# Optimization experiments

Measured on AMD Instinct MI355X. Metric: run time of the kernel, lower is better.

Reference implementation:

```python
import jax, jax.numpy as jnp
import numpy as np

N = 50000      # nodes
F = 128        # in_features
OUT = 128      # out_features
E = 600000     # edges per adjacency (avg degree 12)
J = 2
BN_EPS = 1e-5


def setup_inputs() -> dict:
    key = jax.random.key(0)
    ks = jax.random.split(key, 10)
    x = jax.random.normal(ks[0], (N, F), dtype=jnp.float32)
    rows0 = jax.random.randint(ks[1], (E,), 0, N, dtype=jnp.int32)
    cols0 = jax.random.randint(ks[2], (E,), 0, N, dtype=jnp.int32)
    vals0 = jax.random.uniform(ks[3], (E,), dtype=jnp.float32)
    rows1 = jax.random.randint(ks[4], (E,), 0, N, dtype=jnp.int32)
    cols1 = jax.random.randint(ks[5], (E,), 0, N, dtype=jnp.int32)
    vals1 = jax.random.uniform(ks[6], (E,), dtype=jnp.float32)
    # Linear(J*F, OUT) params, torch default init U(-1/sqrt(fan_in), 1/sqrt(fan_in))
    lim = 1.0 / np.sqrt(J * F)
    W_fc = jax.random.uniform(ks[7], (OUT, J * F), dtype=jnp.float32, minval=-lim, maxval=lim)
    b_fc = jax.random.uniform(ks[8], (OUT,), dtype=jnp.float32, minval=-lim, maxval=lim)
    gamma = jnp.ones((OUT,), dtype=jnp.float32)
    beta = jnp.zeros((OUT,), dtype=jnp.float32)
    return {"x": x, "rows0": rows0, "cols0": cols0, "vals0": vals0,
            "rows1": rows1, "cols1": cols1, "vals1": vals1,
            "W_fc": W_fc, "b_fc": b_fc, "gamma": gamma, "beta": beta}


def _spmm(rows, cols, vals, x):
    # sparse [N,N] @ dense [N,F]: gather source features, weight, scatter-add to rows
    msgs = vals[:, None] * x[cols]                      # [E, F]
    return jax.ops.segment_sum(msgs, rows, num_segments=x.shape[0])  # [N, F]


def reference(x, rows0, cols0, vals0, rows1, cols1, vals1, W_fc, b_fc, gamma, beta):
    h = jnp.concatenate([_spmm(rows0, cols0, vals0, x),
                         _spmm(rows1, cols1, vals1, x)], axis=1)  # [N, J*F]
    y = h @ W_fc.T + b_fc                                         # [N, OUT]
    # BatchNorm1d (training mode: batch stats, biased variance)
    mean = jnp.mean(y, axis=0)
    var = jnp.mean((y - mean) ** 2, axis=0)
    return (y - mean) * jax.lax.rsqrt(var + BN_EPS) * gamma + beta
```

## Files before the change

### kernel.cpp

```cpp
#include <hip/hip_runtime.h>

#define N_NODES 50000
#define F_IN 128
#define OUT_F 128
#define JF 256
#define EDGES 600000
#define BN_EPS 1e-5f
#define MAXDEG 48
#define NPART 8
#define PART_ROWS 6250
#define CHUNK_E 2048
#define NCHUNK 586

#define SCAT_B (NPART * NCHUNK)
#define CONVX_B 6250
#define CONVW_B 32
#define BUILD_B (SCAT_B + CONVX_B + CONVW_B)
#define ROWS_PB 32
#define GATH_B 1563
#define GEMM_ROWS 32
#define GEMM_B 1563
#define HPAD 50048
#define NCOPY 16

typedef __attribute__((ext_vector_type(8))) short short8;
typedef __attribute__((ext_vector_type(4))) float floatx4;
typedef __attribute__((ext_vector_type(4))) unsigned short ushortx4;

static __device__ __forceinline__ unsigned short f2bf(float f) {
    unsigned int x = __float_as_uint(f);
    unsigned int r = (x + 0x7fffu + ((x >> 16) & 1u)) >> 16;
    return (unsigned short)r;
}
static __device__ __forceinline__ float bflo(unsigned int p) { return __uint_as_float(p << 16); }
static __device__ __forceinline__ float bfhi(unsigned int p) { return __uint_as_float(p & 0xffff0000u); }

__global__ __launch_bounds__(256) void build_kernel(
    const int* __restrict__ rows0, const int* __restrict__ cols0, const float* __restrict__ vals0,
    const int* __restrict__ rows1, const int* __restrict__ cols1, const float* __restrict__ vals1,
    int* __restrict__ cnt0, int* __restrict__ cnt1,
    unsigned int* __restrict__ pe0, unsigned int* __restrict__ pe1,
    const floatx4* __restrict__ x4, ushortx4* __restrict__ xb4,
    const float* __restrict__ W, uint2* __restrict__ Wb2)
{
    int bid = blockIdx.x;
    int tid = threadIdx.x;
    if (bid < SCAT_B) {
        unsigned part = (unsigned)(bid & (NPART - 1));
        int c0 = (bid >> 3) * CHUNK_E;

        bool pure0 = (c0 + CHUNK_E <= EDGES);
        bool pure1 = (c0 >= EDGES) && (c0 + CHUNK_E <= 2 * EDGES);
        if (pure0 || pure1) {
            const int*   rows = pure1 ? rows1 : rows0;
            const int*   cols = pure1 ? cols1 : cols0;
            const float* vals = pure1 ? vals1 : vals0;
            int*          cnt = pure1 ? cnt1 : cnt0;
            unsigned int*  pe = pure1 ? pe1 : pe0;
            int eb = pure1 ? c0 - EDGES : c0;
            #pragma unroll
            for (int g = 0; g < 2; ++g) {
                int e = eb + g * 1024 + tid * 4;
                int4 rv = *(const int4*)(rows + e);
                int rr[4] = {rv.x, rv.y, rv.z, rv.w};
                #pragma unroll
                for (int j = 0; j < 4; ++j) {
                    int r = rr[j];
                    if ((unsigned)r / (unsigned)PART_ROWS == part) {
                        int ee = e + j;
                        int c = cols[ee];
                        float v = vals[ee];
                        int p = atomicAdd(&cnt[r], 1);
                        if (p < MAXDEG)
                            pe[(size_t)r * MAXDEG + p] = ((unsigned int)c << 16) | f2bf(v);
                    }
                }
            }
        } else {
            for (int i = 0; i < CHUNK_E / 256; ++i) {
                int e = c0 + i * 256 + tid;
                if (e < 2 * EDGES) {
                    bool s1 = e >= EDGES;
                    int ee = s1 ? e - EDGES : e;
                    int r = s1 ? rows1[ee] : rows0[ee];
                    if ((unsigned)r / (unsigned)PART_ROWS == part) {
                        int c = s1 ? cols1[ee] : cols0[ee];
                        float v = s1 ? vals1[ee] : vals0[ee];
                        int* cnt = s1 ? cnt1 : cnt0;
                        unsigned int* pe = s1 ? pe1 : pe0;
                        int p = atomicAdd(&cnt[r], 1);
                        if (p < MAXDEG)
                            pe[(size_t)r * MAXDEG + p] = ((unsigned int)c << 16) | f2bf(v);
                    }
                }
            }
        }
    } else if (bid < SCAT_B + CONVX_B) {
        int i = (bid - SCAT_B) * 256 + tid;
        floatx4 v = __builtin_nontemporal_load(&x4[i]);
        ushortx4 o;
        o.x = f2bf(v.x); o.y = f2bf(v.y); o.z = f2bf(v.z); o.w = f2bf(v.w);
        __builtin_nontemporal_store(o, &xb4[i]);
    } else {
        int i = (bid - SCAT_B - CONVX_B) * 256 + tid;
        int col = i >> 6, l = i & 63;
        const float* wr = W + (size_t)col * JF;
        float a0 = wr[2 * l], a1 = wr[2 * l + 1];
        float b0 = wr[128 + 2 * l], b1 = wr[128 + 2 * l + 1];
        uint2 o;
        o.x = (unsigned int)f2bf(a0) | ((unsigned int)f2bf(a1) << 16);
        o.y = (unsigned int)f2bf(b0) | ((unsigned int)f2bf(b1) << 16);
        Wb2[col * 64 + l] = o;
    }
}

static __device__ __forceinline__ void rec_u(
    unsigned int q, int lane,
    const unsigned int* __restrict__ xb32, float& A0, float& A1)
{
    unsigned int xv = xb32[(q >> 16) * 64 + lane];
    float vv = __uint_as_float(q << 16);
    A0 += vv * bflo(xv);
    A1 += vv * bfhi(xv);
}
static __device__ __forceinline__ void rec_m(
    unsigned int q, bool on, int lane,
    const unsigned int* __restrict__ xb32, float& A0, float& A1)
{
    unsigned int idx = on ? (q >> 16) : 0u;
    float vv = on ? __uint_as_float(q << 16) : 0.0f;
    unsigned int xv = xb32[idx * 64 + lane];
    A0 += vv * bflo(xv);
    A1 += vv * bfhi(xv);
}

__global__ __launch_bounds__(256, 8) void gather_kernel(
    const unsigned int* __restrict__ xb32,
    const int* __restrict__ cnt0, const unsigned int* __restrict__ pe0,
    const int* __restrict__ cnt1, const unsigned int* __restrict__ pe1,
    uint2* __restrict__ hb)
{
    __shared__ uint4 recs[2][ROWS_PB][6];
    __shared__ int   lcnt[2][ROWS_PB];

    int tid = threadIdx.x;
    int lane = tid & 63;
    int w = tid >> 6;
    int wu = __builtin_amdgcn_readfirstlane(w);
    int row0 = blockIdx.x * ROWS_PB;

    {
        int idx = tid;
        #pragma unroll
        for (int pass = 0; pass < 2; ++pass) {
            if (idx < 384) {
                int lr = idx / 12;
                int rem = idx - lr * 12;
                int side = rem >= 6;
                int g = rem - side * 6;
                int r = row0 + lr; if (r >= N_NODES) r = N_NODES - 1;
                const unsigned int* pe = side ? pe1 : pe0;
                recs[side][lr][g] = *(const uint4*)(pe + (size_t)r * MAXDEG + g * 4);
            }
            idx += 256;
        }
        if (tid < 64) {
            int side = tid >= ROWS_PB;
            int lr = tid & (ROWS_PB - 1);
            int r = row0 + lr;
            int d = 0;
            if (r < N_NODES) d = (side ? cnt1 : cnt0)[r];
            if (d > MAXDEG) d = MAXDEG;
            lcnt[side][lr] = d;
        }
    }
    __syncthreads();

    for (int rr = 0; rr < 8; ++rr) {
        int lr = wu * 8 + rr;
        int r = row0 + lr;
        int d0 = __builtin_amdgcn_readfirstlane(lcnt[0][lr]);
        int d1 = __builtin_amdgcn_readfirstlane(lcnt[1][lr]);

        float aL0 = 0.f, aL1 = 0.f, aR0 = 0.f, aR1 = 0.f;

        #pragma unroll
        for (int g = 0; g < 6; ++g) {
            if (g * 4 < d0) {
                uint4 q = recs[0][lr][g];
                rec_u(q.x, lane, xb32, aL0, aL1);
                rec_m(q.y, g * 4 + 1 < d0, lane, xb32, aL0, aL1);
                rec_m(q.z, g * 4 + 2 < d0, lane, xb32, aL0, aL1);
                rec_m(q.w, g * 4 + 3 < d0, lane, xb32, aL0, aL1);
            }
        }
        #pragma unroll
        for (int g = 0; g < 6; ++g) {
            if (g * 4 < d1) {
                uint4 q = recs[1][lr][g];
                rec_u(q.x, lane, xb32, aR0, aR1);
                rec_m(q.y, g * 4 + 1 < d1, lane, xb32, aR0, aR1);
                rec_m(q.z, g * 4 + 2 < d1, lane, xb32, aR0, aR1);
                rec_m(q.w, g * 4 + 3 < d1, lane, xb32, aR0, aR1);
            }
        }
        if (d0 > 24 && r < N_NODES)
            for (int p = 24; p < d0; ++p)
                rec_u(pe0[(size_t)r * MAXDEG + p], lane, xb32, aL0, aL1);
        if (d1 > 24 && r < N_NODES)
            for (int p = 24; p < d1; ++p)
                rec_u(pe1[(size_t)r * MAXDEG + p], lane, xb32, aR0, aR1);

        uint2 o;
        o.x = (unsigned int)f2bf(aL0) | ((unsigned int)f2bf(aL1) << 16);
        o.y = (unsigned int)f2bf(aR0) | ((unsigned int)f2bf(aR1) << 16);
        hb[(size_t)(row0 + lr) * 64 + lane] = o;
    }
}

__global__ __launch_bounds__(256, 6) void gemm_kernel(
    const char* __restrict__ hb,
    const ushort* __restrict__ Wb,
    const float* __restrict__ bias,
    float* __restrict__ y, float* __restrict__ stats)
{
    __shared__ float lstat[256];

    int tid = threadIdx.x;
    int lane = tid & 63;
    int w = tid >> 6;
    int row0 = blockIdx.x * GEMM_ROWS + (w & 1) * 16;
    int cbase = (w >> 1) * 64;

    lstat[tid] = 0.f;
    __syncthreads();

    int colb = lane & 15;
    int kg = lane >> 4;
    const char* abase = hb + (size_t)(row0 + colb) * 512 + kg * 16;

    floatx4 acc[4];
    #pragma unroll
    for (int c = 0; c < 4; ++c) acc[c] = (floatx4){0.f, 0.f, 0.f, 0.f};

    #pragma unroll
    for (int k0 = 0; k0 < 8; ++k0) {
        short8 a = *(const short8*)(abase + k0 * 64);
        #pragma unroll
        for (int c = 0; c < 4; ++c) {
            short8 b = *(const short8*)(Wb + (size_t)(cbase + c * 16 + colb) * 256 + k0 * 32 + kg * 8);
            acc[c] = __builtin_amdgcn_mfma_f32_16x16x32_bf16(a, b, acc[c], 0, 0, 0);
        }
    }

    #pragma unroll
    for (int c = 0; c < 4; ++c) {
        int col = cbase + c * 16 + colb;
        float bv = bias[col];
        float s = 0.f, s2 = 0.f;
        #pragma unroll
        for (int q = 0; q < 4; ++q) {
            int row = row0 + kg * 4 + q;
            if (row < N_NODES) {
                float val = acc[c][q] + bv;
                y[(size_t)row * OUT_F + col] = val;
                s += val; s2 += val * val;
            }
        }
        atomicAdd(&lstat[col], s);
        atomicAdd(&lstat[128 + col], s2);
    }
    __syncthreads();
    float* sdst = stats + (size_t)(blockIdx.x & (NCOPY - 1)) * 256;
    atomicAdd(&sdst[tid], lstat[tid]);
}

__global__ void bn_prep(const float* __restrict__ stats,
                        const float* __restrict__ gamma,
                        const float* __restrict__ beta,
                        float* __restrict__ ss)
{
    int o = threadIdx.x;
    if (o >= OUT_F) return;
    float s = 0.f, s2 = 0.f;
    #pragma unroll
    for (int c = 0; c < NCOPY; ++c) {
        s  += stats[c * 256 + o];
        s2 += stats[c * 256 + 128 + o];
    }
    float inv_n = 1.0f / (float)N_NODES;
    float mean = s * inv_n;
    float var  = s2 * inv_n - mean * mean;
    float sc = rsqrtf(var + BN_EPS) * gamma[o];
    ss[o] = sc;
    ss[OUT_F + o] = beta[o] - mean * sc;
}

__global__ __launch_bounds__(256) void bn_apply(
    float* __restrict__ y, const float* __restrict__ ss)
{
    size_t i = (size_t)blockIdx.x * blockDim.x + threadIdx.x;
    size_t total = (size_t)N_NODES * OUT_F / 4;
    if (i >= total) return;

    int c4 = (int)(i & (OUT_F / 4 - 1));
    float4 v  = ((const float4*)y)[i];
    float4 sc = ((const float4*)ss)[c4];
    float4 sh = ((const float4*)(ss + OUT_F))[c4];
    v.x = v.x * sc.x + sh.x;
    v.y = v.y * sc.y + sh.y;
    v.z = v.z * sc.z + sh.z;
    v.w = v.w * sc.w + sh.w;
    ((float4*)y)[i] = v;
}

extern "C" void kernel_launch(void* const* d_in, const int* in_sizes, int n_in,
                              void* d_out, int out_size, void* d_ws, size_t ws_size,
                              hipStream_t stream)
{
    const float* x     = (const float*)d_in[0];
    const int*   rows0 = (const int*)  d_in[1];
    const int*   cols0 = (const int*)  d_in[2];
    const float* vals0 = (const float*)d_in[3];
    const int*   rows1 = (const int*)  d_in[4];
    const int*   cols1 = (const int*)  d_in[5];
    const float* vals1 = (const float*)d_in[6];
    const float* W     = (const float*)d_in[7];
    const float* b     = (const float*)d_in[8];
    const float* gamma = (const float*)d_in[9];
    const float* beta  = (const float*)d_in[10];

    float* y = (float*)d_out;

    ushort* xb = (ushort*)d_ws;
    ushort* Wb = xb + (size_t)N_NODES * F_IN;
    unsigned int* pe0 = (unsigned int*)(Wb + OUT_F * JF);
    unsigned int* pe1 = pe0 + (size_t)N_NODES * MAXDEG;
    uint2* hb = (uint2*)(pe1 + (size_t)N_NODES * MAXDEG);
    int* cnt0 = (int*)(hb + (size_t)HPAD * 64);
    int* cnt1 = cnt0 + N_NODES;
    float* stats = (float*)(cnt1 + N_NODES);
    float* ss    = stats + NCOPY * 256;

    hipMemsetAsync(cnt0, 0,
                   (2 * (size_t)N_NODES + NCOPY * 256) * sizeof(int),
                   stream);

    build_kernel<<<BUILD_B, 256, 0, stream>>>(
        rows0, cols0, vals0, rows1, cols1, vals1,
        cnt0, cnt1, pe0, pe1,
        (const floatx4*)x, (ushortx4*)xb, W, (uint2*)Wb);

    gather_kernel<<<GATH_B, 256, 0, stream>>>(
        (const unsigned int*)xb, cnt0, pe0, cnt1, pe1, hb);

    gemm_kernel<<<GEMM_B, 256, 0, stream>>>(
        (const char*)hb, Wb, b, y, stats);

    bn_prep<<<1, 128, 0, stream>>>(stats, gamma, beta, ss);
    bn_apply<<<CONVX_B, 256, 0, stream>>>(y, ss);
}
```

Baseline: 170.2 us.

## Pre-pack edges into compact arrays before partitioned scatter; fuse BN prep into apply

Adds a prep pass that packs row indices into 16-bit values and packs col/val pairs into one 32-bit word per edge. A separate scatter kernel then has each of the 8 partition blocks read the compact row array, so the repeated row scans across partitions read half the bytes and the col/val loads become a single word. The one-block bn_prep launch is merged into bn_apply: every block recomputes the scale and shift in shared memory. This costs an extra kernel launch and an extra pass writing and reading the packed arrays, and each bn block redoes the small stats reduction.

```diff
diff --git a/kernel.cpp b/kernel.cpp
--- a/kernel.cpp
+++ b/kernel.cpp
@@ -12,10 +12,12 @@
 #define CHUNK_E 2048
 #define NCHUNK 586
 
-#define SCAT_B (NPART * NCHUNK)
+#define RPACK_B 586
+#define EV_B 1172
 #define CONVX_B 6250
 #define CONVW_B 32
-#define BUILD_B (SCAT_B + CONVX_B + CONVW_B)
+#define PREP_B (RPACK_B + EV_B + CONVX_B + CONVW_B)
+#define SCAT_B (NPART * NCHUNK)
 #define ROWS_PB 32
 #define GATH_B 1563
 #define GEMM_ROWS 32
@@ -24,6 +26,7 @@
 #define NCOPY 16
 
 typedef __attribute__((ext_vector_type(8))) short short8;
+typedef __attribute__((ext_vector_type(8))) unsigned short ushortx8;
 typedef __attribute__((ext_vector_type(4))) float floatx4;
 typedef __attribute__((ext_vector_type(4))) unsigned short ushortx4;
 
@@ -35,74 +38,52 @@
 static __device__ __forceinline__ float bflo(unsigned int p) { return __uint_as_float(p << 16); }
 static __device__ __forceinline__ float bfhi(unsigned int p) { return __uint_as_float(p & 0xffff0000u); }
 
-__global__ __launch_bounds__(256) void build_kernel(
+__global__ __launch_bounds__(256) void prep_kernel(
     const int* __restrict__ rows0, const int* __restrict__ cols0, const float* __restrict__ vals0,
     const int* __restrict__ rows1, const int* __restrict__ cols1, const float* __restrict__ vals1,
-    int* __restrict__ cnt0, int* __restrict__ cnt1,
-    unsigned int* __restrict__ pe0, unsigned int* __restrict__ pe1,
+    unsigned short* __restrict__ rpack, unsigned int* __restrict__ ev,
     const floatx4* __restrict__ x4, ushortx4* __restrict__ xb4,
     const float* __restrict__ W, uint2* __restrict__ Wb2)
 {
     int bid = blockIdx.x;
     int tid = threadIdx.x;
-    if (bid < SCAT_B) {
-        unsigned part = (unsigned)(bid & (NPART - 1));
-        int c0 = (bid >> 3) * CHUNK_E;
-
-        bool pure0 = (c0 + CHUNK_E <= EDGES);
-        bool pure1 = (c0 >= EDGES) && (c0 + CHUNK_E <= 2 * EDGES);
-        if (pure0 || pure1) {
-            const int*   rows = pure1 ? rows1 : rows0;
-            const int*   cols = pure1 ? cols1 : cols0;
-            const float* vals = pure1 ? vals1 : vals0;
-            int*          cnt = pure1 ? cnt1 : cnt0;
-            unsigned int*  pe = pure1 ? pe1 : pe0;
-            int eb = pure1 ? c0 - EDGES : c0;
-            #pragma unroll
-            for (int g = 0; g < 2; ++g) {
-                int e = eb + g * 1024 + tid * 4;
-                int4 rv = *(const int4*)(rows + e);
-                int rr[4] = {rv.x, rv.y, rv.z, rv.w};
-                #pragma unroll
-                for (int j = 0; j < 4; ++j) {
-                    int r = rr[j];
-                    if ((unsigned)r / (unsigned)PART_ROWS == part) {
-                        int ee = e + j;
-                        int c = cols[ee];
-                        float v = vals[ee];
-                        int p = atomicAdd(&cnt[r], 1);
-                        if (p < MAXDEG)
-                            pe[(size_t)r * MAXDEG + p] = ((unsigned int)c << 16) | f2bf(v);
-                    }
-                }
-            }
-        } else {
-            for (int i = 0; i < CHUNK_E / 256; ++i) {
-                int e = c0 + i * 256 + tid;
-                if (e < 2 * EDGES) {
-                    bool s1 = e >= EDGES;
-                    int ee = s1 ? e - EDGES : e;
-                    int r = s1 ? rows1[ee] : rows0[ee];
-                    if ((unsigned)r / (unsigned)PART_ROWS == part) {
-                        int c = s1 ? cols1[ee] : cols0[ee];
-                        float v = s1 ? vals1[ee] : vals0[ee];
-                        int* cnt = s1 ? cnt1 : cnt0;
-                        unsigned int* pe = s1 ? pe1 : pe0;
-                        int p = atomicAdd(&cnt[r], 1);
-                        if (p < MAXDEG)
-                            pe[(size_t)r * MAXDEG + p] = ((unsigned int)c << 16) | f2bf(v);
-                    }
-                }
-            }
-        }
-    } else if (bid < SCAT_B + CONVX_B) {
-        int i = (bid - SCAT_B) * 256 + tid;
+    if (bid < RPACK_B) {
+        int e0 = bid * 2048 + tid * 8;
+        if (e0 < 2 * EDGES) {
+            bool s1 = e0 >= EDGES;
+            const int* rows = s1 ? rows1 : rows0;
+            int eb = s1 ? e0 - EDGES : e0;
+            int4 a = *(const int4*)(rows + eb);
+            int4 b = *(const int4*)(rows + eb + 4);
+            ushortx8 o;
+            o.s0 = (unsigned short)a.x; o.s1 = (unsigned short)a.y;
+            o.s2 = (unsigned short)a.z; o.s3 = (unsigned short)a.w;
+            o.s4 = (unsigned short)b.x; o.s5 = (unsigned short)b.y;
+            o.s6 = (unsigned short)b.z; o.s7 = (unsigned short)b.w;
+            *(ushortx8*)(rpack + e0) = o;
+        }
+    } else if (bid < RPACK_B + EV_B) {
+        int e0 = (bid - RPACK_B) * 1024 + tid * 4;
+        if (e0 < 2 * EDGES) {
+            bool s1 = e0 >= EDGES;
+            int eb = s1 ? e0 - EDGES : e0;
+            int4 c = *(const int4*)((s1 ? cols1 : cols0) + eb);
+            float4 v = *(const float4*)((s1 ? vals1 : vals0) + eb);
+            uint4 o;
+            o.x = ((unsigned)c.x << 16) | f2bf(v.x);
+            o.y = ((unsigned)c.y << 16) | f2bf(v.y);
+            o.z = ((unsigned)c.z << 16) | f2bf(v.z);
+            o.w = ((unsigned)c.w << 16) | f2bf(v.w);
+            *(uint4*)(ev + e0) = o;
+        }
+    } else if (bid < RPACK_B + EV_B + CONVX_B) {
+        int i = (bid - RPACK_B - EV_B) * 256 + tid;
         floatx4 v = __builtin_nontemporal_load(&x4[i]);
         ushortx4 o;
         o.x = f2bf(v.x); o.y = f2bf(v.y); o.z = f2bf(v.z); o.w = f2bf(v.w);
         __builtin_nontemporal_store(o, &xb4[i]);
     } else {
-        int i = (bid - SCAT_B - CONVX_B) * 256 + tid;
+        int i = (bid - RPACK_B - EV_B - CONVX_B) * 256 + tid;
         int col = i >> 6, l = i & 63;
         const float* wr = W + (size_t)col * JF;
         float a0 = wr[2 * l], a1 = wr[2 * l + 1];
@@ -111,6 +92,33 @@
         o.x = (unsigned int)f2bf(a0) | ((unsigned int)f2bf(a1) << 16);
         o.y = (unsigned int)f2bf(b0) | ((unsigned int)f2bf(b1) << 16);
         Wb2[col * 64 + l] = o;
+    }
+}
+
+__global__ __launch_bounds__(256) void scat_kernel(
+    const unsigned short* __restrict__ rpack, const unsigned int* __restrict__ ev,
+    int* __restrict__ cnt0, int* __restrict__ cnt1,
+    unsigned int* __restrict__ pe0, unsigned int* __restrict__ pe1)
+{
+    unsigned part = (unsigned)(blockIdx.x & (NPART - 1));
+    int e0 = (blockIdx.x >> 3) * CHUNK_E + threadIdx.x * 8;
+    if (e0 >= 2 * EDGES) return;
+
+    bool s1 = e0 >= EDGES;
+    int* __restrict__ cnt = s1 ? cnt1 : cnt0;
+    unsigned int* __restrict__ pe = s1 ? pe1 : pe0;
+
+    ushortx8 rp = *(const ushortx8*)(rpack + e0);
+    unsigned rr[8] = {rp.s0, rp.s1, rp.s2, rp.s3, rp.s4, rp.s5, rp.s6, rp.s7};
+    #pragma unroll
+    for (int j = 0; j < 8; ++j) {
+        unsigned r = rr[j];
+        if (r / (unsigned)PART_ROWS == part) {
+            unsigned q = ev[e0 + j];
+            int p = atomicAdd(&cnt[r], 1);
+            if (p < MAXDEG)
+                pe[(size_t)r * MAXDEG + p] = q;
+        }
     }
 }
 
@@ -275,42 +283,40 @@
     atomicAdd(&sdst[tid], lstat[tid]);
 }
 
-__global__ void bn_prep(const float* __restrict__ stats,
-                        const float* __restrict__ gamma,
-                        const float* __restrict__ beta,
-                        float* __restrict__ ss)
-{
-    int o = threadIdx.x;
-    if (o >= OUT_F) return;
-    float s = 0.f, s2 = 0.f;
-    #pragma unroll
-    for (int c = 0; c < NCOPY; ++c) {
-        s  += stats[c * 256 + o];
-        s2 += stats[c * 256 + 128 + o];
-    }
-    float inv_n = 1.0f / (float)N_NODES;
-    float mean = s * inv_n;
-    float var  = s2 * inv_n - mean * mean;
-    float sc = rsqrtf(var + BN_EPS) * gamma[o];
-    ss[o] = sc;
-    ss[OUT_F + o] = beta[o] - mean * sc;
-}
-
 __global__ __launch_bounds__(256) void bn_apply(
-    float* __restrict__ y, const float* __restrict__ ss)
-{
-    size_t i = (size_t)blockIdx.x * blockDim.x + threadIdx.x;
+    float* __restrict__ y,
+    const float* __restrict__ stats,
+    const float* __restrict__ gamma,
+    const float* __restrict__ beta)
+{
+    __shared__ float ssl[256];
+    int tid = threadIdx.x;
+    if (tid < OUT_F) {
+        float s = 0.f, s2 = 0.f;
+        #pragma unroll
+        for (int c = 0; c < NCOPY; ++c) {
+            s  += stats[c * 256 + tid];
+            s2 += stats[c * 256 + 128 + tid];
+        }
+        float inv_n = 1.0f / (float)N_NODES;
+        float mean = s * inv_n;
+        float var  = s2 * inv_n - mean * mean;
+        float sc = rsqrtf(var + BN_EPS) * gamma[tid];
+        ssl[tid] = sc;
+        ssl[128 + tid] = beta[tid] - mean * sc;
+    }
+    __syncthreads();
+
+    size_t i = (size_t)blockIdx.x * blockDim.x + tid;
     size_t total = (size_t)N_NODES * OUT_F / 4;
     if (i >= total) return;
 
     int c4 = (int)(i & (OUT_F / 4 - 1));
-    float4 v  = ((const float4*)y)[i];
-    float4 sc = ((const float4*)ss)[c4];
-    float4 sh = ((const float4*)(ss + OUT_F))[c4];
-    v.x = v.x * sc.x + sh.x;
-    v.y = v.y * sc.y + sh.y;
-    v.z = v.z * sc.z + sh.z;
-    v.w = v.w * sc.w + sh.w;
+    float4 v = ((const float4*)y)[i];
+    v.x = v.x * ssl[4 * c4 + 0] + ssl[128 + 4 * c4 + 0];
+    v.y = v.y * ssl[4 * c4 + 1] + ssl[128 + 4 * c4 + 1];
+    v.z = v.z * ssl[4 * c4 + 2] + ssl[128 + 4 * c4 + 2];
+    v.w = v.w * ssl[4 * c4 + 3] + ssl[128 + 4 * c4 + 3];
     ((float4*)y)[i] = v;
 }
 
@@ -337,19 +343,22 @@
     unsigned int* pe0 = (unsigned int*)(Wb + OUT_F * JF);
     unsigned int* pe1 = pe0 + (size_t)N_NODES * MAXDEG;
     uint2* hb = (uint2*)(pe1 + (size_t)N_NODES * MAXDEG);
-    int* cnt0 = (int*)(hb + (size_t)HPAD * 64);
+    unsigned short* rpack = (unsigned short*)(hb + (size_t)HPAD * 64);
+    unsigned int* ev = (unsigned int*)(rpack + 2 * EDGES + 128);
+    int* cnt0 = (int*)(ev + 2 * EDGES);
     int* cnt1 = cnt0 + N_NODES;
     float* stats = (float*)(cnt1 + N_NODES);
-    float* ss    = stats + NCOPY * 256;
 
     hipMemsetAsync(cnt0, 0,
                    (2 * (size_t)N_NODES + NCOPY * 256) * sizeof(int),
                    stream);
 
-    build_kernel<<<BUILD_B, 256, 0, stream>>>(
+    prep_kernel<<<PREP_B, 256, 0, stream>>>(
         rows0, cols0, vals0, rows1, cols1, vals1,
-        cnt0, cnt1, pe0, pe1,
+        rpack, ev,
         (const floatx4*)x, (ushortx4*)xb, W, (uint2*)Wb);
+
+    scat_kernel<<<SCAT_B, 256, 0, stream>>>(rpack, ev, cnt0, cnt1, pe0, pe1);
 
     gather_kernel<<<GATH_B, 256, 0, stream>>>(
         (const unsigned int*)xb, cnt0, pe0, cnt1, pe1, hb);
@@ -357,6 +366,5 @@
     gemm_kernel<<<GEMM_B, 256, 0, stream>>>(
         (const char*)hb, Wb, b, y, stats);
 
-    bn_prep<<<1, 128, 0, stream>>>(stats, gamma, beta, ss);
-    bn_apply<<<CONVX_B, 256, 0, stream>>>(y, ss);
-}
+    bn_apply<<<CONVX_B, 256, 0, stream>>>(y, stats, gamma, beta);
+}
```

Result: no change. 173.5 us (+1.9%).
